# Kernel optimization log

Hardware: AMD Instinct MI355X
Metric: run time of the kernel (lower is better)

## Reference

```python
import jax, jax.numpy as jnp
import numpy as np

D_MODEL = 1024
N_HEADS = 16
D_K = D_MODEL // N_HEADS
B, S = 2, 2048


def setup_inputs() -> dict:
    key = jax.random.key(0)
    ks = jax.random.split(key, 12)
    scale = 1.0 / np.sqrt(D_MODEL)
    inp = {
        "query": jax.random.normal(ks[0], (B, S, D_MODEL), jnp.float32),
        "key": jax.random.normal(ks[1], (B, S, D_MODEL), jnp.float32),
        "value": jax.random.normal(ks[2], (B, S, D_MODEL), jnp.float32),
        "mask": jnp.tril(jnp.ones((S, S), dtype=bool))[None, None],  # (1,1,S,S) causal
        "W_q": jax.random.normal(ks[3], (D_MODEL, D_MODEL), jnp.float32) * scale,
        "b_q": jnp.zeros((D_MODEL,), jnp.float32),
        "W_k": jax.random.normal(ks[4], (D_MODEL, D_MODEL), jnp.float32) * scale,
        "b_k": jnp.zeros((D_MODEL,), jnp.float32),
        "W_v": jax.random.normal(ks[5], (D_MODEL, D_MODEL), jnp.float32) * scale,
        "b_v": jnp.zeros((D_MODEL,), jnp.float32),
        "W_o": jax.random.normal(ks[6], (D_MODEL, D_MODEL), jnp.float32) * scale,
        "b_o": jnp.zeros((D_MODEL,), jnp.float32),
    }
    return inp


def reference(query, key, value, mask, W_q, b_q, W_k, b_k, W_v, b_v, W_o, b_o):
    b = query.shape[0]
    # Linear projections (torch Linear: x @ W.T + b), split into heads -> (b,h,s,d_k)
    def proj(x, W, bias):
        y = x @ W.T + bias
        return y.reshape(b, -1, N_HEADS, D_K).transpose(0, 2, 1, 3)

    q = proj(query, W_q, b_q)
    k = proj(key, W_k, b_k)
    v = proj(value, W_v, b_v)

    # scores: (b,h,sq,sk)
    scores = jnp.einsum("bhqd,bhkd->bhqk", q, k) / jnp.sqrt(jnp.float32(D_K)).astype(q.dtype)
    scores = jnp.where(mask, scores, jnp.finfo(scores.dtype).min)
    attn = jax.nn.softmax(scores, axis=-1)
    out = jnp.einsum("bhqk,bhkd->bhqd", attn, v)  # (b,h,sq,d_k)
    out = out.transpose(0, 2, 1, 3).reshape(b, -1, D_MODEL)
    return out @ W_o.T + b_o
```

## Files before the change

kernel.cpp:

```cpp
#include <hip/hip_runtime.h>
#include <hip/hip_bf16.h>
#include <stdint.h>

#define D_MODEL 1024
#define NH 16
#define DK 64
#define BB 2
#define SS 2048
#define MROWS (BB*SS)

typedef __attribute__((ext_vector_type(8))) short bf16x8;
typedef __attribute__((ext_vector_type(4))) float f32x4;

__device__ __forceinline__ short to_bf16(float f) {
  __hip_bfloat16 h = __float2bfloat16(f);
  union { __hip_bfloat16 b; short s; } u; u.b = h; return u.s;
}

__device__ __forceinline__ f32x4 mfma16(bf16x8 a, bf16x8 b, f32x4 c) {
  return __builtin_amdgcn_mfma_f32_16x16x32_bf16(a, b, c, 0, 0, 0);
}

__device__ __forceinline__ void gload_lds16(const void* g, void* l) {
  __builtin_amdgcn_global_load_lds(
      (const __attribute__((address_space(1))) unsigned int*)g,
      (__attribute__((address_space(3))) unsigned int*)l,
      16, 0, 0);
}

__global__ __launch_bounds__(256) void cvt3(const float* __restrict__ a,
                                            const float* __restrict__ b,
                                            const float* __restrict__ c,
                                            short* __restrict__ oa,
                                            short* __restrict__ ob,
                                            short* __restrict__ oc) {
  const int z = blockIdx.z;
  const float* x = z == 0 ? a : z == 1 ? b : c;
  short* y = z == 0 ? oa : z == 1 ? ob : oc;
  const int i = (blockIdx.x * 256 + threadIdx.x) * 4;
  const float4 v = *(const float4*)(x + i);
  short4 o;
  o.x = to_bf16(v.x); o.y = to_bf16(v.y); o.z = to_bf16(v.z); o.w = to_bf16(v.w);
  *(short4*)(y + i) = o;
}

__global__ __launch_bounds__(256) void cvt4(const float* __restrict__ a,
                                            const float* __restrict__ b,
                                            const float* __restrict__ c,
                                            const float* __restrict__ d,
                                            short* __restrict__ oa,
                                            short* __restrict__ ob,
                                            short* __restrict__ oc,
                                            short* __restrict__ od) {
  const int z = blockIdx.z;
  const float* x = z == 0 ? a : z == 1 ? b : z == 2 ? c : d;
  short* y = z == 0 ? oa : z == 1 ? ob : z == 2 ? oc : od;
  const int i = (blockIdx.x * 256 + threadIdx.x) * 4;
  const float4 v = *(const float4*)(x + i);
  short4 o;
  o.x = to_bf16(v.x); o.y = to_bf16(v.y); o.z = to_bf16(v.z); o.w = to_bf16(v.w);
  *(short4*)(y + i) = o;
}

__global__ __launch_bounds__(256) void gemm_qkv(const short* __restrict__ Xq,
                                                const short* __restrict__ Xk,
                                                const short* __restrict__ Xv,
                                                const short* __restrict__ Wq,
                                                const short* __restrict__ Wk,
                                                const short* __restrict__ Wv,
                                                const float* __restrict__ bq,
                                                const float* __restrict__ bk,
                                                const float* __restrict__ bv,
                                                short* __restrict__ Qh,
                                                short* __restrict__ Kh,
                                                short* __restrict__ VT) {
  constexpr int K = 1024;
  __shared__ short As[128 * 64];
  __shared__ short Bs[128 * 64];
  const int z = blockIdx.z;
  const short* A    = z == 0 ? Xq : z == 1 ? Xk : Xv;
  const short* Wt   = z == 0 ? Wq : z == 1 ? Wk : Wv;
  const float* bias = z == 0 ? bq : z == 1 ? bk : bv;

  const int tid = threadIdx.x;
  const int w = tid >> 6, lane = tid & 63;
  const int m0 = blockIdx.x * 128, n0 = blockIdx.y * 128;
  const int wm = w >> 1, wn = w & 1;
  const int fr = lane & 15, fg = lane >> 4;
  const int srow = tid >> 3, scol = (tid & 7) * 8;

  f32x4 acc[4][4] = {};

  for (int k0 = 0; k0 < K; k0 += 64) {
    __syncthreads();
#pragma unroll
    for (int i = 0; i < 4; ++i) {
      const int row = i * 32 + srow;
      gload_lds16(A  + (size_t)(m0 + row) * K + k0 + scol, As + row * 64 + scol);
      gload_lds16(Wt + (size_t)(n0 + row) * K + k0 + scol, Bs + row * 64 + scol);
    }
    asm volatile("s_waitcnt vmcnt(0)" ::: "memory");
    __syncthreads();

    bf16x8 af[4][2], bfr[4][2];
#pragma unroll
    for (int i = 0; i < 4; ++i)
#pragma unroll
      for (int hh = 0; hh < 2; ++hh) {
        af[i][hh]  = *(const bf16x8*)(As + (wm * 64 + i * 16 + fr) * 64 + hh * 32 + fg * 8);
        bfr[i][hh] = *(const bf16x8*)(Bs + (wn * 64 + i * 16 + fr) * 64 + hh * 32 + fg * 8);
      }
    __builtin_amdgcn_s_setprio(1);
#pragma unroll
    for (int mi = 0; mi < 4; ++mi)
#pragma unroll
      for (int ni = 0; ni < 4; ++ni) {
        acc[mi][ni] = mfma16(af[mi][0], bfr[ni][0], acc[mi][ni]);
        acc[mi][ni] = mfma16(af[mi][1], bfr[ni][1], acc[mi][ni]);
      }
    __builtin_amdgcn_s_setprio(0);
  }

  const float scale = (z == 0) ? 0.18033688011112042f : 1.0f;
#pragma unroll
  for (int mi = 0; mi < 4; ++mi)
#pragma unroll
    for (int ni = 0; ni < 4; ++ni) {
      const int col = n0 + wn * 64 + ni * 16 + fr;
      const float bval = bias[col];
      const int h = col >> 6, d = col & 63;
#pragma unroll
      for (int r = 0; r < 4; ++r) {
        const int row = m0 + wm * 64 + mi * 16 + fg * 4 + r;
        const float val = (acc[mi][ni][r] + bval) * scale;
        const int b = row >> 11, s = row & (SS - 1);
        if (z < 2) {
          short* dst = (z == 0) ? Qh : Kh;
          dst[((size_t)(b * NH + h) * SS + s) * DK + d] = to_bf16(val);
        } else {
          VT[((size_t)(b * NH + h) * DK + d) * SS + s] = to_bf16(val);
        }
      }
    }
}

__global__ __launch_bounds__(256) void gemm_out(const short* __restrict__ A,
                                                const short* __restrict__ Wt,
                                                const float* __restrict__ bias,
                                                float* __restrict__ Y) {
  constexpr int K = 1024;
  __shared__ short As[128 * 64];
  __shared__ short Bs[64 * 64];
  const int tid = threadIdx.x;
  const int w = tid >> 6, lane = tid & 63;
  const int m0 = blockIdx.x * 128, n0 = blockIdx.y * 64;
  const int wm = w >> 1, wn = w & 1;
  const int fr = lane & 15, fg = lane >> 4;
  const int srow = tid >> 3, scol = (tid & 7) * 8;

  f32x4 acc[4][2] = {};

  for (int k0 = 0; k0 < K; k0 += 64) {
    __syncthreads();
#pragma unroll
    for (int i = 0; i < 4; ++i) {
      const int row = i * 32 + srow;
      gload_lds16(A + (size_t)(m0 + row) * K + k0 + scol, As + row * 64 + scol);
    }
#pragma unroll
    for (int i = 0; i < 2; ++i) {
      const int row = i * 32 + srow;
      gload_lds16(Wt + (size_t)(n0 + row) * K + k0 + scol, Bs + row * 64 + scol);
    }
    asm volatile("s_waitcnt vmcnt(0)" ::: "memory");
    __syncthreads();

    bf16x8 af[4][2], bfr[2][2];
#pragma unroll
    for (int i = 0; i < 4; ++i)
#pragma unroll
      for (int hh = 0; hh < 2; ++hh)
        af[i][hh] = *(const bf16x8*)(As + (wm * 64 + i * 16 + fr) * 64 + hh * 32 + fg * 8);
#pragma unroll
    for (int i = 0; i < 2; ++i)
#pragma unroll
      for (int hh = 0; hh < 2; ++hh)
        bfr[i][hh] = *(const bf16x8*)(Bs + (wn * 32 + i * 16 + fr) * 64 + hh * 32 + fg * 8);
    __builtin_amdgcn_s_setprio(1);
#pragma unroll
    for (int mi = 0; mi < 4; ++mi)
#pragma unroll
      for (int ni = 0; ni < 2; ++ni) {
        acc[mi][ni] = mfma16(af[mi][0], bfr[ni][0], acc[mi][ni]);
        acc[mi][ni] = mfma16(af[mi][1], bfr[ni][1], acc[mi][ni]);
      }
    __builtin_amdgcn_s_setprio(0);
  }

#pragma unroll
  for (int mi = 0; mi < 4; ++mi)
#pragma unroll
    for (int ni = 0; ni < 2; ++ni) {
      const int col = n0 + wn * 32 + ni * 16 + fr;
      const float bval = bias[col];
#pragma unroll
      for (int r = 0; r < 4; ++r) {
        const int row = m0 + wm * 64 + mi * 16 + fg * 4 + r;
        Y[(size_t)row * D_MODEL + col] = acc[mi][ni][r] + bval;
      }
    }
}

__global__ __launch_bounds__(256, 4) void attn_kernel(const short* __restrict__ Qh,
                                                      const short* __restrict__ Kh,
                                                      const short* __restrict__ VT,
                                                      short* __restrict__ AO) {
  __shared__ short Ks[2][64 * 64];
  __shared__ short Vs[2][64 * 64];
  __shared__ short P_lds[4][16 * 64];

  const int tid = threadIdx.x, w = tid >> 6, lane = tid & 63;
  const int fr = lane & 15, fg = lane >> 4;
  const int kr = fg * 4;
  const int swz = (fr & 7) << 4;

  const int bid = blockIdx.x;
  const int lid = ((bid & 7) << 7) | (bid >> 3);
  const int bh = lid >> 5;
  const int idx = lid & 31;
  const int P = (idx & 1) ? (31 - (idx >> 1)) : (idx >> 1);
  const int b = bh >> 4, h = bh & 15;
  const int qw = P * 64 + w * 16;

  const short* Qp = Qh + (size_t)bh * SS * DK;
  const short* Kp = Kh + (size_t)bh * SS * DK;
  const short* Vp = VT + (size_t)bh * DK * SS;

  const int sc_c = tid & 7;
  const int sc_r = tid >> 3;

  bf16x8 qf[2];
#pragma unroll
  for (int hh = 0; hh < 2; ++hh)
    qf[hh] = *(const bf16x8*)(Qp + (size_t)(qw + fr) * DK + hh * 32 + fg * 8);

  const short onev = (fr == 0) ? (short)0x3F80 : (short)0;
  const bf16x8 af4 = {onev, onev, onev, onev, onev, onev, onev, onev};

  f32x4 o[5] = {};
  float m_run = -1e30f;

  const int T = P + 1;

#define STAGE_KV(buf, t0)                                                     \
  do {                                                                        \
    const int kk0 = (t0) * 64;                                                \
    _Pragma("unroll") for (int p = 0; p < 2; ++p) {                           \
      const int row = p * 32 + sc_r;                                          \
      const int sc = sc_c ^ (row & 7);                                        \
      gload_lds16(Kp + (size_t)(kk0 + row) * DK + sc * 8,                     \
                  &Ks[buf][row * 64 + sc_c * 8]);                             \
      gload_lds16(Vp + (size_t)row * SS + kk0 + sc * 8,                       \
                  &Vs[buf][row * 64 + sc_c * 8]);                             \
    }                                                                         \
  } while (0)

  STAGE_KV(0, 0);
  asm volatile("s_waitcnt vmcnt(0)" ::: "memory");
  __syncthreads();

  for (int ti = 0; ti < T; ++ti) {
    const int cur = ti & 1;
    if (ti + 1 < T) STAGE_KV(cur ^ 1, ti + 1);

    const char* KsB = (const char*)Ks[cur];
    const char* VsB = (const char*)Vs[cur];

    f32x4 st[4];
    __builtin_amdgcn_s_setprio(1);
#pragma unroll
    for (int kt = 0; kt < 4; ++kt) {
      const bf16x8 k0f = *(const bf16x8*)(KsB + (kt * 16 + fr) * 128 + ((fg * 16) ^ swz));
      const bf16x8 k1f = *(const bf16x8*)(KsB + (kt * 16 + fr) * 128 + ((64 + fg * 16) ^ swz));
      f32x4 z = {};
      z = mfma16(k0f, qf[0], z);
      z = mfma16(k1f, qf[1], z);
      st[kt] = z;
    }
    __builtin_amdgcn_s_setprio(0);

    if (ti == T - 1) {
#pragma unroll
      for (int kt = 0; kt < 4; ++kt)
#pragma unroll
        for (int r = 0; r < 4; ++r)
          if (kt * 16 + kr + r > w * 16 + fr) st[kt][r] = -1e30f;
    }

    float pmax = st[0][0];
#pragma unroll
    for (int kt = 0; kt < 4; ++kt)
#pragma unroll
      for (int r = 0; r < 4; ++r) pmax = fmaxf(pmax, st[kt][r]);
    pmax = fmaxf(pmax, __shfl_xor(pmax, 16));
    pmax = fmaxf(pmax, __shfl_xor(pmax, 32));

    if (!__all(pmax <= m_run + 11.0f)) {
      const float mn = fmaxf(m_run, pmax);
      const float al = __builtin_amdgcn_exp2f(m_run - mn);
      m_run = mn;
#pragma unroll
      for (int t = 0; t < 5; ++t)
#pragma unroll
        for (int r = 0; r < 4; ++r) o[t][r] *= al;
    }

    {
      char* base = (char*)P_lds[w];
#pragma unroll
      for (int kt = 0; kt < 4; ++kt) {
        short4 sv;
        sv.x = to_bf16(__builtin_amdgcn_exp2f(st[kt][0] - m_run));
        sv.y = to_bf16(__builtin_amdgcn_exp2f(st[kt][1] - m_run));
        sv.z = to_bf16(__builtin_amdgcn_exp2f(st[kt][2] - m_run));
        sv.w = to_bf16(__builtin_amdgcn_exp2f(st[kt][3] - m_run));
        *(short4*)(base + ((fr * 128 + kt * 32 + fg * 8) ^ swz)) = sv;
      }
    }
    asm volatile("s_waitcnt lgkmcnt(0)" ::: "memory");

    __builtin_amdgcn_s_setprio(1);
#pragma unroll
    for (int c = 0; c < 2; ++c) {
      const bf16x8 pf = *(const bf16x8*)((const char*)P_lds[w] +
                                         ((fr * 128 + c * 64 + fg * 16) ^ swz));
#pragma unroll
      for (int t = 0; t < 4; ++t) {
        const bf16x8 vfb = *(const bf16x8*)(VsB + (t * 16 + fr) * 128 +
                                            ((c * 64 + fg * 16) ^ swz));
        o[t] = mfma16(vfb, pf, o[t]);
      }
      o[4] = mfma16(af4, pf, o[4]);
    }
    __builtin_amdgcn_s_setprio(0);

    asm volatile("s_waitcnt vmcnt(0)" ::: "memory");
    __syncthreads();
  }
#undef STAGE_KV

  const float l = __shfl(o[4][0], fr);
  const float inv = 1.0f / l;
  const int s = qw + fr;
#pragma unroll
  for (int t = 0; t < 4; ++t) {
    short4 ov = {to_bf16(o[t][0] * inv), to_bf16(o[t][1] * inv),
                 to_bf16(o[t][2] * inv), to_bf16(o[t][3] * inv)};
    *(short4*)(AO + (size_t)(b * SS + s) * D_MODEL + h * 64 + t * 16 + kr) = ov;
  }
}

extern "C" void kernel_launch(void* const* d_in, const int* in_sizes, int n_in,
                              void* d_out, int out_size, void* d_ws, size_t ws_size,
                              hipStream_t stream) {
  const float* q  = (const float*)d_in[0];
  const float* k  = (const float*)d_in[1];
  const float* v  = (const float*)d_in[2];
  const float* Wq = (const float*)d_in[4];
  const float* bq = (const float*)d_in[5];
  const float* Wk = (const float*)d_in[6];
  const float* bk = (const float*)d_in[7];
  const float* Wv = (const float*)d_in[8];
  const float* bv = (const float*)d_in[9];
  const float* Wo = (const float*)d_in[10];
  const float* bo = (const float*)d_in[11];

  char* ws = (char*)d_ws;
  const size_t MB = 1u << 20;
  short* Xq = (short*)(ws + 0 * MB);
  short* Xk = (short*)(ws + 8 * MB);
  short* Xv = (short*)(ws + 16 * MB);
  short* Bq = (short*)(ws + 24 * MB);
  short* Bk = (short*)(ws + 26 * MB);
  short* Bv = (short*)(ws + 28 * MB);
  short* Bo = (short*)(ws + 30 * MB);
  short* Qh = (short*)(ws + 32 * MB);
  short* Kh = (short*)(ws + 40 * MB);
  short* VT = (short*)(ws + 48 * MB);
  short* AO = (short*)(ws + 56 * MB);

  cvt3<<<dim3(MROWS * D_MODEL / 1024, 1, 3), 256, 0, stream>>>(q, k, v, Xq, Xk, Xv);
  cvt4<<<dim3(D_MODEL * D_MODEL / 1024, 1, 4), 256, 0, stream>>>(Wq, Wk, Wv, Wo, Bq, Bk, Bv, Bo);

  gemm_qkv<<<dim3(MROWS / 128, D_MODEL / 128, 3), 256, 0, stream>>>(
      Xq, Xk, Xv, Bq, Bk, Bv, bq, bk, bv, Qh, Kh, VT);

  attn_kernel<<<dim3(1024), 256, 0, stream>>>(Qh, Kh, VT, AO);

  gemm_out<<<dim3(MROWS / 128, D_MODEL / 64), 256, 0, stream>>>(AO, Bo, bo, (float*)d_out);
}
```

Measured before the change: 133.9 us.

## Pair causal query tiles per block to balance attention work

Each attention block now handles two query tiles, j and 31-j, so every block walks exactly 33 key tiles in one continuous pipelined loop. The grid is halved to 512 blocks. After the first tile it writes the output, resets the accumulators and loads the second Q fragment. This is meant to remove load imbalance and tail effects from uneven causal tile lengths, at the cost of fewer blocks and lower occupancy, since the launch-bounds minimum of 4 blocks is dropped.

```diff
diff --git a/kernel.cpp b/kernel.cpp
--- a/kernel.cpp
+++ b/kernel.cpp
@@ -211,10 +211,10 @@
     }
 }
 
-__global__ __launch_bounds__(256, 4) void attn_kernel(const short* __restrict__ Qh,
-                                                      const short* __restrict__ Kh,
-                                                      const short* __restrict__ VT,
-                                                      short* __restrict__ AO) {
+__global__ __launch_bounds__(256) void attn_kernel(const short* __restrict__ Qh,
+                                                   const short* __restrict__ Kh,
+                                                   const short* __restrict__ VT,
+                                                   short* __restrict__ AO) {
   __shared__ short Ks[2][64 * 64];
   __shared__ short Vs[2][64 * 64];
   __shared__ short P_lds[4][16 * 64];
@@ -225,12 +225,10 @@
   const int swz = (fr & 7) << 4;
 
   const int bid = blockIdx.x;
-  const int lid = ((bid & 7) << 7) | (bid >> 3);
-  const int bh = lid >> 5;
-  const int idx = lid & 31;
-  const int P = (idx & 1) ? (31 - (idx >> 1)) : (idx >> 1);
+  const int lid = ((bid & 7) << 6) | (bid >> 3);
+  const int bh = lid >> 4;
+  const int j = lid & 15;
   const int b = bh >> 4, h = bh & 15;
-  const int qw = P * 64 + w * 16;
 
   const short* Qp = Qh + (size_t)bh * SS * DK;
   const short* Kp = Kh + (size_t)bh * SS * DK;
@@ -239,6 +237,9 @@
   const int sc_c = tid & 7;
   const int sc_r = tid >> 3;
 
+  const int T0 = j + 1;
+
+  int qw = j * 64 + w * 16;
   bf16x8 qf[2];
 #pragma unroll
   for (int hh = 0; hh < 2; ++hh)
@@ -250,17 +251,14 @@
   f32x4 o[5] = {};
   float m_run = -1e30f;
 
-  const int T = P + 1;
-
-#define STAGE_KV(buf, t0)                                                     \
+#define STAGE_KV(buf, kk0)                                                    \
   do {                                                                        \
-    const int kk0 = (t0) * 64;                                                \
     _Pragma("unroll") for (int p = 0; p < 2; ++p) {                           \
       const int row = p * 32 + sc_r;                                          \
       const int sc = sc_c ^ (row & 7);                                        \
-      gload_lds16(Kp + (size_t)(kk0 + row) * DK + sc * 8,                     \
+      gload_lds16(Kp + (size_t)((kk0) + row) * DK + sc * 8,                   \
                   &Ks[buf][row * 64 + sc_c * 8]);                             \
-      gload_lds16(Vp + (size_t)row * SS + kk0 + sc * 8,                       \
+      gload_lds16(Vp + (size_t)row * SS + (kk0) + sc * 8,                     \
                   &Vs[buf][row * 64 + sc_c * 8]);                             \
     }                                                                         \
   } while (0)
@@ -269,9 +267,12 @@
   asm volatile("s_waitcnt vmcnt(0)" ::: "memory");
   __syncthreads();
 
-  for (int ti = 0; ti < T; ++ti) {
-    const int cur = ti & 1;
-    if (ti + 1 < T) STAGE_KV(cur ^ 1, ti + 1);
+  for (int g = 0; g < 33; ++g) {
+    const int cur = g & 1;
+    if (g + 1 < 33) {
+      const int nk0 = (g + 1 < T0) ? (g + 1) * 64 : (g + 1 - T0) * 64;
+      STAGE_KV(cur ^ 1, nk0);
+    }
 
     const char* KsB = (const char*)Ks[cur];
     const char* VsB = (const char*)Vs[cur];
@@ -289,7 +290,7 @@
     }
     __builtin_amdgcn_s_setprio(0);
 
-    if (ti == T - 1) {
+    if (g == T0 - 1 || g == 32) {
 #pragma unroll
       for (int kt = 0; kt < 4; ++kt)
 #pragma unroll
@@ -346,6 +347,27 @@
 
     asm volatile("s_waitcnt vmcnt(0)" ::: "memory");
     __syncthreads();
+
+    if (g == T0 - 1) {
+      const float l = __shfl(o[4][0], fr);
+      const float inv = 1.0f / l;
+      const int s = qw + fr;
+#pragma unroll
+      for (int t = 0; t < 4; ++t) {
+        short4 ov = {to_bf16(o[t][0] * inv), to_bf16(o[t][1] * inv),
+                     to_bf16(o[t][2] * inv), to_bf16(o[t][3] * inv)};
+        *(short4*)(AO + (size_t)(b * SS + s) * D_MODEL + h * 64 + t * 16 + kr) = ov;
+      }
+#pragma unroll
+      for (int t = 0; t < 5; ++t)
+#pragma unroll
+        for (int r = 0; r < 4; ++r) o[t][r] = 0.f;
+      m_run = -1e30f;
+      qw = (31 - j) * 64 + w * 16;
+#pragma unroll
+      for (int hh = 0; hh < 2; ++hh)
+        qf[hh] = *(const bf16x8*)(Qp + (size_t)(qw + fr) * DK + hh * 32 + fg * 8);
+    }
   }
 #undef STAGE_KV
 
@@ -395,7 +417,7 @@
   gemm_qkv<<<dim3(MROWS / 128, D_MODEL / 128, 3), 256, 0, stream>>>(
       Xq, Xk, Xv, Bq, Bk, Bv, bq, bk, bv, Qh, Kh, VT);
 
-  attn_kernel<<<dim3(1024), 256, 0, stream>>>(Qh, Kh, VT, AO);
+  attn_kernel<<<dim3(512), 256, 0, stream>>>(Qh, Kh, VT, AO);
 
   gemm_out<<<dim3(MROWS / 128, D_MODEL / 64), 256, 0, stream>>>(AO, Bo, bo, (float*)d_out);
 }
```

After: 126.2 us. 5.8% less time.
